# Kernel optimization log

Hardware: AMD Instinct MI355X
Metric: run time of the kernel (lower is better)

## Reference

```python
import math
import jax, jax.numpy as jnp
import numpy as np

EMB = 1024
HEADS = 16
HEAD_DIM = EMB // HEADS


def setup_inputs() -> dict:
    key = jax.random.key(0)
    ks = jax.random.split(key, 6)
    b, l = 4, 4096
    x = jax.random.normal(ks[0], (b, l, EMB), dtype=jnp.float32)
    # torch Linear weight shape (out, in); xavier_normal std = sqrt(2/(in+out))
    std = math.sqrt(2.0 / (EMB + EMB))
    Wq = jax.random.normal(ks[1], (EMB, EMB), dtype=jnp.float32) * std
    Wk = jax.random.normal(ks[2], (EMB, EMB), dtype=jnp.float32) * std
    Wv = jax.random.normal(ks[3], (EMB, EMB), dtype=jnp.float32) * std
    Wu = jax.random.normal(ks[4], (EMB, EMB), dtype=jnp.float32) * std
    Wo = jax.random.normal(ks[5], (EMB, EMB), dtype=jnp.float32) * std
    return {"x": x, "Wq": Wq, "Wk": Wk, "Wv": Wv, "Wu": Wu, "Wo": Wo}


def _srms_norm(x, eps=1e-12):
    # SRMSNorm over last dim with scale 1/sqrt(head_dims), computed in fp32
    dtype = x.dtype
    xf = x.astype(jnp.float32)
    scale = 1.0 / math.sqrt(x.shape[-1])
    n = jnp.linalg.norm(xf * scale, axis=-1, keepdims=True)
    return (xf / jnp.maximum(n, eps)).astype(dtype)


def reference(x, Wq, Wk, Wv, Wu, Wo):
    b, l, d = x.shape
    h, hd = HEADS, HEAD_DIM
    scale = math.sqrt(hd)

    def proj(W):
        return jnp.einsum('bld,ed->ble', x, W).reshape(b, l, h, hd).transpose(0, 2, 1, 3)

    q = jax.nn.relu(proj(Wq)) / scale        # (b,h,l,hd)
    k = jax.nn.relu(proj(Wk)) / scale
    v = proj(Wv)
    u = jax.nn.silu(proj(Wu))

    kv = jnp.einsum('bhlk,bhlv->bhkv', k, v)  # (b,h,hd,hd) state
    out = jnp.einsum('bhlk,bhkv->bhlv', q, kv)
    out = _srms_norm(out) * u
    out = out.transpose(0, 2, 1, 3).reshape(b, l, d)
    return jnp.einsum('bld,ed->ble', out, Wo)
```

## Files before the change

### kernel.cpp

```cpp
#include <hip/hip_runtime.h>

typedef _Float16 f16;
typedef _Float16 f16x4 __attribute__((ext_vector_type(4)));
typedef _Float16 f16x8 __attribute__((ext_vector_type(8)));
typedef float f32x4 __attribute__((ext_vector_type(4)));

#define EMB 1024
#define SEQL 4096
#define BATCH 4
#define NH 16
#define HD 64
#define BH 64
#define MROWS 16384
#define KVSPLIT 16

#define GLOAD_LDS(gp, lp) \
    __builtin_amdgcn_global_load_lds((const __attribute__((address_space(1))) void*)(gp), \
                                     (__attribute__((address_space(3))) void*)(lp), 16, 0, 0)

__global__ void cvt_kernel(const float* __restrict__ in, f16* __restrict__ out, int n4) {
    int i = blockIdx.x * blockDim.x + threadIdx.x;
    if (i < n4) {
        float4 v = ((const float4*)in)[i];
        f16x4 o = { (f16)v.x, (f16)v.y, (f16)v.z, (f16)v.w };
        ((f16x4*)out)[i] = o;
    }
}

struct WPtrs { const float* p[5]; };

__global__ void cvt_w_kernel(WPtrs wp, f16* __restrict__ out) {
    int i = blockIdx.x * blockDim.x + threadIdx.x;
    int wsel = blockIdx.y;
    const float4* src = (const float4*)wp.p[wsel];
    float4 v = src[i];
    f16x4 o = { (f16)v.x, (f16)v.y, (f16)v.z, (f16)v.w };
    ((f16x4*)(out + (size_t)wsel * EMB * EMB))[i] = o;
}

__global__ void zero_kernel(float4* __restrict__ p, int n4) {
    int i = blockIdx.x * blockDim.x + threadIdx.x;
    if (i < n4) p[i] = float4{0.f, 0.f, 0.f, 0.f};
}

template<int MODE>
__global__ __launch_bounds__(256) void gemm_kernel(
    const f16* __restrict__ A, const f16* __restrict__ Bt,
    void* __restrict__ Cv, int M, int N, int K)
{
    __shared__ f16 As[128 * 32];
    __shared__ f16 Bs[128 * 32];

    const int lane = threadIdx.x & 63;
    const int w    = threadIdx.x >> 6;
    const int rw   = lane & 15;
    const int quad = lane >> 4;
    const int m0 = blockIdx.y * 128;
    const int n0 = blockIdx.x * 128;
    const int mw = (w >> 1) * 64;
    const int nw = (w & 1) * 64;

    const int srow = lane >> 2;
    const int scol = (((lane & 3) ^ ((lane >> 3) & 3)) * 8);
    const f16* ag0 = A  + (size_t)(m0 + w * 16 + srow) * K + scol;
    const f16* ag1 = A  + (size_t)(m0 + 64 + w * 16 + srow) * K + scol;
    const f16* bg0 = Bt + (size_t)(n0 + w * 16 + srow) * K + scol;
    const f16* bg1 = Bt + (size_t)(n0 + 64 + w * 16 + srow) * K + scol;
    f16* la0 = &As[(w * 16) * 32];
    f16* la1 = &As[(64 + w * 16) * 32];
    f16* lb0 = &Bs[(w * 16) * 32];
    f16* lb1 = &Bs[(64 + w * 16) * 32];

    const int swz = (quad ^ ((rw >> 1) & 3)) * 8;

    f32x4 acc[4][4] = {};

    for (int k0 = 0; k0 < K; k0 += 32) {
        __syncthreads();
        GLOAD_LDS(ag0 + k0, la0);
        GLOAD_LDS(ag1 + k0, la1);
        GLOAD_LDS(bg0 + k0, lb0);
        GLOAD_LDS(bg1 + k0, lb1);
        __syncthreads();

        f16x8 af[4], bf[4];
        #pragma unroll
        for (int i = 0; i < 4; i++)
            af[i] = *(const f16x8*)&As[(mw + 16 * i + rw) * 32 + swz];
        #pragma unroll
        for (int j = 0; j < 4; j++)
            bf[j] = *(const f16x8*)&Bs[(nw + 16 * j + rw) * 32 + swz];
        #pragma unroll
        for (int i = 0; i < 4; i++)
            #pragma unroll
            for (int j = 0; j < 4; j++)
                acc[i][j] = __builtin_amdgcn_mfma_f32_16x16x32_f16(bf[j], af[i], acc[i][j], 0, 0, 0);
    }

    #pragma unroll
    for (int i = 0; i < 4; i++) {
        #pragma unroll
        for (int j = 0; j < 4; j++) {
            const int m_idx = m0 + mw + 16 * i + rw;
            const int n_idx = n0 + nw + 16 * j + quad * 4;
            if (MODE == 0) {
                float4 vv = { acc[i][j][0], acc[i][j][1], acc[i][j][2], acc[i][j][3] };
                *(float4*)&((float*)Cv)[(size_t)m_idx * N + n_idx] = vv;
            } else if (MODE == 3) {
                int sel = n_idx >> 10, e = n_idx & 1023;
                int b = m_idx >> 12, l = m_idx & 4095, h = e >> 6, hd = e & 63;
                f16x4 o;
                #pragma unroll
                for (int r = 0; r < 4; r++) {
                    float v = acc[i][j][r];
                    o[r] = (f16)(sel ? (v / (1.0f + __expf(-v))) : (fmaxf(v, 0.0f) * 0.125f));
                }
                *(f16x4*)&((f16*)Cv)[(size_t)sel * MROWS * EMB +
                                     (((size_t)(b * 16 + h) * 4096 + l) << 6) + hd] = o;
            } else {
                int sel = m_idx >> 10, e = m_idx & 1023;
                int b = n_idx >> 12, l = n_idx & 4095;
                f16x4 o;
                #pragma unroll
                for (int r = 0; r < 4; r++) {
                    float v = acc[i][j][r];
                    o[r] = (f16)(sel ? v : (fmaxf(v, 0.0f) * 0.125f));
                }
                *(f16x4*)&((f16*)Cv)[(size_t)sel * MROWS * EMB +
                                     (((size_t)b * 1024 + e) << 12) + l] = o;
            }
        }
    }
}

__global__ __launch_bounds__(256) void kv_split_kernel(
    const f16* __restrict__ kT, const f16* __restrict__ vT, float* __restrict__ kv32)
{
    const int bh    = blockIdx.x;
    const int chunk = blockIdx.y;
    const int lane  = threadIdx.x & 63;
    const int w     = threadIdx.x >> 6;
    const int rw    = lane & 15;
    const int quad  = lane >> 4;
    const int lbase = chunk * (SEQL / KVSPLIT);

    const f16* kp = kT + (size_t)bh * HD * SEQL + (size_t)(w * 16 + rw) * SEQL + lbase + quad * 8;
    const f16* vp = vT + (size_t)bh * HD * SEQL + (size_t)rw * SEQL + lbase + quad * 8;

    f32x4 acc[4] = {};
    for (int k0 = 0; k0 < SEQL / KVSPLIT; k0 += 32) {
        f16x8 a = *(const f16x8*)(kp + k0);
        #pragma unroll
        for (int t = 0; t < 4; t++) {
            f16x8 b = *(const f16x8*)(vp + (size_t)16 * t * SEQL + k0);
            acc[t] = __builtin_amdgcn_mfma_f32_16x16x32_f16(a, b, acc[t], 0, 0, 0);
        }
    }
    float* out = kv32 + (size_t)bh * HD * HD;
    #pragma unroll
    for (int t = 0; t < 4; t++)
        #pragma unroll
        for (int r = 0; r < 4; r++)
            atomicAdd(&out[(w * 16 + quad * 4 + r) * 64 + t * 16 + rw], acc[t][r]);
}

__global__ __launch_bounds__(256) void ret_out_kernel(
    const f16* __restrict__ q, const f16* __restrict__ u,
    const float* __restrict__ kv32, f16* __restrict__ o)
{
    const int bh    = blockIdx.x;
    const int chunk = blockIdx.y;
    const int lane  = threadIdx.x & 63;
    const int w     = threadIdx.x >> 6;
    const int rw    = lane & 15;
    const int quad  = lane >> 4;

    const float* kvp = kv32 + (size_t)bh * 4096;
    f16x8 bf[2][4];
    #pragma unroll
    for (int s = 0; s < 2; s++)
        #pragma unroll
        for (int t = 0; t < 4; t++)
            #pragma unroll
            for (int j = 0; j < 8; j++)
                bf[s][t][j] = (f16)kvp[(s * 32 + quad * 8 + j) * 64 + t * 16 + rw];

    const f16* qp = q + (size_t)bh * SEQL * HD;
    const f16* up = u + (size_t)bh * SEQL * HD;
    const int b = bh >> 4, h = bh & 15;
    f16* op = o + (size_t)b * SEQL * EMB + h * 64;

    const int l_wave = chunk * 512 + w * 128;
    for (int s = 0; s < 8; s++) {
        const int l0 = l_wave + s * 16;
        f16x8 a0 = *(const f16x8*)(qp + (size_t)(l0 + rw) * 64 + quad * 8);
        f16x8 a1 = *(const f16x8*)(qp + (size_t)(l0 + rw) * 64 + 32 + quad * 8);
        f32x4 acc[4] = {};
        #pragma unroll
        for (int t = 0; t < 4; t++) {
            acc[t] = __builtin_amdgcn_mfma_f32_16x16x32_f16(a0, bf[0][t], acc[t], 0, 0, 0);
            acc[t] = __builtin_amdgcn_mfma_f32_16x16x32_f16(a1, bf[1][t], acc[t], 0, 0, 0);
        }
        float inv[4];
        #pragma unroll
        for (int r = 0; r < 4; r++) {
            float ss = acc[0][r] * acc[0][r] + acc[1][r] * acc[1][r]
                     + acc[2][r] * acc[2][r] + acc[3][r] * acc[3][r];
            #pragma unroll
            for (int msk = 1; msk < 16; msk <<= 1)
                ss += __shfl_xor(ss, msk, 16);
            inv[r] = 8.0f / fmaxf(sqrtf(ss), 8e-12f);
        }
        #pragma unroll
        for (int t = 0; t < 4; t++)
            #pragma unroll
            for (int r = 0; r < 4; r++) {
                int l = l0 + quad * 4 + r;
                int col = t * 16 + rw;
                float uval = (float)up[(size_t)l * 64 + col];
                op[(size_t)l * EMB + col] = (f16)(acc[t][r] * inv[r] * uval);
            }
    }
}

extern "C" void kernel_launch(void* const* d_in, const int* in_sizes, int n_in,
                              void* d_out, int out_size, void* d_ws, size_t ws_size,
                              hipStream_t stream)
{
    const float* x = (const float*)d_in[0];
    WPtrs wp;
    wp.p[0] = (const float*)d_in[1];
    wp.p[1] = (const float*)d_in[4];
    wp.p[2] = (const float*)d_in[2];
    wp.p[3] = (const float*)d_in[3];
    wp.p[4] = (const float*)d_in[5];

    char* ws = (char*)d_ws;
    size_t off = 0;
    f16* x16 = (f16*)(ws + off); off += (size_t)MROWS * EMB * 2;
    f16* w16 = (f16*)(ws + off); off += (size_t)5 * EMB * EMB * 2;
    f16* qb  = (f16*)(ws + off); off += (size_t)MROWS * EMB * 2;
    f16* ub  = (f16*)(ws + off); off += (size_t)MROWS * EMB * 2;
    f16* kTb = (f16*)(ws + off); off += (size_t)MROWS * EMB * 2;
    f16* vTb = (f16*)(ws + off); off += (size_t)MROWS * EMB * 2;
    float* kv32 = (float*)(ws + off); off += (size_t)BH * HD * HD * 4;
    f16* ob  = x16;
    (void)ub; (void)vTb;

    cvt_kernel<<<(MROWS * EMB / 4) / 256, 256, 0, stream>>>(x, x16, MROWS * EMB / 4);
    cvt_w_kernel<<<dim3((EMB * EMB / 4) / 256, 5), 256, 0, stream>>>(wp, w16);
    zero_kernel<<<(BH * HD * HD / 4 + 255) / 256, 256, 0, stream>>>((float4*)kv32, BH * HD * HD / 4);

    f16* Wqu = w16;
    f16* Wkv = w16 + (size_t)2 * EMB * EMB;
    f16* Wo  = w16 + (size_t)4 * EMB * EMB;

    dim3 blk(256);
    gemm_kernel<3><<<dim3(16, 128), blk, 0, stream>>>(x16, Wqu, qb, MROWS, 2 * EMB, EMB);
    gemm_kernel<4><<<dim3(128, 16), blk, 0, stream>>>(Wkv, x16, kTb, 2 * EMB, MROWS, EMB);

    kv_split_kernel<<<dim3(BH, KVSPLIT), blk, 0, stream>>>(kTb, vTb, kv32);
    ret_out_kernel<<<dim3(BH, 8), blk, 0, stream>>>(qb, ub, kv32, ob);

    gemm_kernel<0><<<dim3(8, 128), blk, 0, stream>>>(ob, Wo, d_out, MROWS, EMB, EMB);
}
```

Measured before the change: 449.3 us.

## Fuse QU/KV projections into one GEMM with per-wave private LDS prefetch

Merges the two projection GEMMs into a single launch over the concatenated Wq/Wk/Wv/Wu weights. For the K/V half it swaps the MFMA operand order, so the transposed layout comes straight out of the accumulators. The GEMM is restructured so each wave stages its own 64-row A and B slices into private LDS regions. This replaces block-wide __syncthreads with waitcnt-based software prefetch of the next k-tile, overlapping global loads with MFMA. In exchange, each wave reloads operand rows that other waves also load, which raises global/L2 traffic. Waves also now depend on manual waitcnt encodings for correctness.

```diff
diff --git a/kernel.cpp b/kernel.cpp
--- a/kernel.cpp
+++ b/kernel.cpp
@@ -18,6 +18,9 @@
     __builtin_amdgcn_global_load_lds((const __attribute__((address_space(1))) void*)(gp), \
                                      (__attribute__((address_space(3))) void*)(lp), 16, 0, 0)
 
+#define WAIT_VM0   0x0F70
+#define WAIT_LGKM0 0xC07F
+
 __global__ void cvt_kernel(const float* __restrict__ in, f16* __restrict__ out, int n4) {
     int i = blockIdx.x * blockDim.x + threadIdx.x;
     if (i < n4) {
@@ -44,69 +47,91 @@
 }
 
 template<int MODE>
-__global__ __launch_bounds__(256) void gemm_kernel(
+__global__ __launch_bounds__(256) void gemmw_kernel(
     const f16* __restrict__ A, const f16* __restrict__ Bt,
-    void* __restrict__ Cv, int M, int N, int K)
-{
-    __shared__ f16 As[128 * 32];
-    __shared__ f16 Bs[128 * 32];
+    void* __restrict__ C0, void* __restrict__ Ckv, int M, int N, int K)
+{
+    __shared__ f16 SA[4 * 2048];
+    __shared__ f16 SB[4 * 2048];
 
     const int lane = threadIdx.x & 63;
     const int w    = threadIdx.x >> 6;
     const int rw   = lane & 15;
     const int quad = lane >> 4;
-    const int m0 = blockIdx.y * 128;
-    const int n0 = blockIdx.x * 128;
-    const int mw = (w >> 1) * 64;
-    const int nw = (w & 1) * 64;
+
+    const int nb  = (MODE == 1) ? 32 : 8;
+    const int lin = blockIdx.x;
+    const int m0  = (lin / nb) * 128;
+    const int n0  = (lin % nb) * 128;
+    const int mw  = (w >> 1) * 64;
+    const int nw  = (w & 1) * 64;
+    const bool kvhalf = (MODE == 1) && ((n0 + nw) >= 2048);
 
     const int srow = lane >> 2;
     const int scol = (((lane & 3) ^ ((lane >> 3) & 3)) * 8);
-    const f16* ag0 = A  + (size_t)(m0 + w * 16 + srow) * K + scol;
-    const f16* ag1 = A  + (size_t)(m0 + 64 + w * 16 + srow) * K + scol;
-    const f16* bg0 = Bt + (size_t)(n0 + w * 16 + srow) * K + scol;
-    const f16* bg1 = Bt + (size_t)(n0 + 64 + w * 16 + srow) * K + scol;
-    f16* la0 = &As[(w * 16) * 32];
-    f16* la1 = &As[(64 + w * 16) * 32];
-    f16* lb0 = &Bs[(w * 16) * 32];
-    f16* lb1 = &Bs[(64 + w * 16) * 32];
+    const f16* a_src = A  + (size_t)(m0 + mw + srow) * K + scol;
+    const f16* b_src = Bt + (size_t)(n0 + nw + srow) * K + scol;
+    f16* lA = &SA[w * 2048];
+    f16* lB = &SB[w * 2048];
 
     const int swz = (quad ^ ((rw >> 1) & 3)) * 8;
 
+    auto stage = [&](int k0) {
+        #pragma unroll
+        for (int g = 0; g < 4; g++)
+            GLOAD_LDS(a_src + (size_t)(g * 16) * K + k0, lA + g * 512);
+        #pragma unroll
+        for (int g = 0; g < 4; g++)
+            GLOAD_LDS(b_src + (size_t)(g * 16) * K + k0, lB + g * 512);
+    };
+
     f32x4 acc[4][4] = {};
+    stage(0);
 
     for (int k0 = 0; k0 < K; k0 += 32) {
-        __syncthreads();
-        GLOAD_LDS(ag0 + k0, la0);
-        GLOAD_LDS(ag1 + k0, la1);
-        GLOAD_LDS(bg0 + k0, lb0);
-        GLOAD_LDS(bg1 + k0, lb1);
-        __syncthreads();
-
+        __builtin_amdgcn_s_waitcnt(WAIT_VM0);
         f16x8 af[4], bf[4];
         #pragma unroll
         for (int i = 0; i < 4; i++)
-            af[i] = *(const f16x8*)&As[(mw + 16 * i + rw) * 32 + swz];
+            af[i] = *(const f16x8*)&lA[(16 * i + rw) * 32 + swz];
         #pragma unroll
         for (int j = 0; j < 4; j++)
-            bf[j] = *(const f16x8*)&Bs[(nw + 16 * j + rw) * 32 + swz];
-        #pragma unroll
-        for (int i = 0; i < 4; i++)
-            #pragma unroll
-            for (int j = 0; j < 4; j++)
-                acc[i][j] = __builtin_amdgcn_mfma_f32_16x16x32_f16(bf[j], af[i], acc[i][j], 0, 0, 0);
-    }
-
-    #pragma unroll
-    for (int i = 0; i < 4; i++) {
-        #pragma unroll
-        for (int j = 0; j < 4; j++) {
-            const int m_idx = m0 + mw + 16 * i + rw;
-            const int n_idx = n0 + nw + 16 * j + quad * 4;
-            if (MODE == 0) {
+            bf[j] = *(const f16x8*)&lB[(16 * j + rw) * 32 + swz];
+        __builtin_amdgcn_s_waitcnt(WAIT_LGKM0);
+        if (k0 + 32 < K) stage(k0 + 32);
+
+        if (kvhalf) {
+            #pragma unroll
+            for (int i = 0; i < 4; i++)
+                #pragma unroll
+                for (int j = 0; j < 4; j++)
+                    acc[i][j] = __builtin_amdgcn_mfma_f32_16x16x32_f16(af[i], bf[j], acc[i][j], 0, 0, 0);
+        } else {
+            #pragma unroll
+            for (int i = 0; i < 4; i++)
+                #pragma unroll
+                for (int j = 0; j < 4; j++)
+                    acc[i][j] = __builtin_amdgcn_mfma_f32_16x16x32_f16(bf[j], af[i], acc[i][j], 0, 0, 0);
+        }
+    }
+
+    if (MODE == 0) {
+        #pragma unroll
+        for (int i = 0; i < 4; i++)
+            #pragma unroll
+            for (int j = 0; j < 4; j++) {
+                const int m_idx = m0 + mw + 16 * i + rw;
+                const int n_idx = n0 + nw + 16 * j + quad * 4;
                 float4 vv = { acc[i][j][0], acc[i][j][1], acc[i][j][2], acc[i][j][3] };
-                *(float4*)&((float*)Cv)[(size_t)m_idx * N + n_idx] = vv;
-            } else if (MODE == 3) {
+                *(float4*)&((float*)C0)[(size_t)m_idx * N + n_idx] = vv;
+            }
+    } else if (!kvhalf) {
+        #pragma unroll
+        for (int i = 0; i < 4; i++)
+            #pragma unroll
+            for (int j = 0; j < 4; j++) {
+                const int m_idx = m0 + mw + 16 * i + rw;
+                const int n_idx = n0 + nw + 16 * j + quad * 4;
                 int sel = n_idx >> 10, e = n_idx & 1023;
                 int b = m_idx >> 12, l = m_idx & 4095, h = e >> 6, hd = e & 63;
                 f16x4 o;
@@ -115,21 +140,27 @@
                     float v = acc[i][j][r];
                     o[r] = (f16)(sel ? (v / (1.0f + __expf(-v))) : (fmaxf(v, 0.0f) * 0.125f));
                 }
-                *(f16x4*)&((f16*)Cv)[(size_t)sel * MROWS * EMB +
+                *(f16x4*)&((f16*)C0)[(size_t)sel * MROWS * EMB +
                                      (((size_t)(b * 16 + h) * 4096 + l) << 6) + hd] = o;
-            } else {
-                int sel = m_idx >> 10, e = m_idx & 1023;
-                int b = n_idx >> 12, l = n_idx & 4095;
+            }
+    } else {
+        #pragma unroll
+        for (int i = 0; i < 4; i++)
+            #pragma unroll
+            for (int j = 0; j < 4; j++) {
+                const int n_idx = n0 + nw + 16 * j + rw - 2048;
+                const int m_idx = m0 + mw + 16 * i + quad * 4;
+                int sel = n_idx >> 10, e = n_idx & 1023;
+                int b = m_idx >> 12, l = m_idx & 4095;
                 f16x4 o;
                 #pragma unroll
                 for (int r = 0; r < 4; r++) {
                     float v = acc[i][j][r];
                     o[r] = (f16)(sel ? v : (fmaxf(v, 0.0f) * 0.125f));
                 }
-                *(f16x4*)&((f16*)Cv)[(size_t)sel * MROWS * EMB +
-                                     (((size_t)b * 1024 + e) << 12) + l] = o;
-            }
-        }
+                *(f16x4*)&((f16*)Ckv)[(size_t)sel * MROWS * EMB +
+                                      (((size_t)b * 1024 + e) << 12) + l] = o;
+            }
     }
 }
 
@@ -251,16 +282,14 @@
     cvt_w_kernel<<<dim3((EMB * EMB / 4) / 256, 5), 256, 0, stream>>>(wp, w16);
     zero_kernel<<<(BH * HD * HD / 4 + 255) / 256, 256, 0, stream>>>((float4*)kv32, BH * HD * HD / 4);
 
-    f16* Wqu = w16;
-    f16* Wkv = w16 + (size_t)2 * EMB * EMB;
-    f16* Wo  = w16 + (size_t)4 * EMB * EMB;
+    f16* Wqukv = w16;
+    f16* Wo    = w16 + (size_t)4 * EMB * EMB;
 
     dim3 blk(256);
-    gemm_kernel<3><<<dim3(16, 128), blk, 0, stream>>>(x16, Wqu, qb, MROWS, 2 * EMB, EMB);
-    gemm_kernel<4><<<dim3(128, 16), blk, 0, stream>>>(Wkv, x16, kTb, 2 * EMB, MROWS, EMB);
+    gemmw_kernel<1><<<dim3(128 * 32), blk, 0, stream>>>(x16, Wqukv, qb, kTb, MROWS, 4 * EMB, EMB);
 
     kv_split_kernel<<<dim3(BH, KVSPLIT), blk, 0, stream>>>(kTb, vTb, kv32);
     ret_out_kernel<<<dim3(BH, 8), blk, 0, stream>>>(qb, ub, kv32, ob);
 
-    gemm_kernel<0><<<dim3(8, 128), blk, 0, stream>>>(ob, Wo, d_out, MROWS, EMB, EMB);
-}
+    gemmw_kernel<0><<<dim3(128 * 8), blk, 0, stream>>>(ob, Wo, d_out, nullptr, MROWS, EMB, EMB);
+}
```

Result: slower. 528.0 us (+17.5%).
